# Optimization experiments

Hardware: AMD Instinct MI355X
Metric: run time of the kernel (lower is better)

Reference implementation:

```python
import jax, jax.numpy as jnp
import numpy as np

B, N, K, IN, H, D = 4, 4096, 32, 64, 4, 64  # batch, nodes, max degree, in_dim, heads, out_dim
HD = H * D
NEG_SLOPE = 0.2
EPS = 1e-5


def setup_inputs() -> dict:
    key = jax.random.key(0)
    ks = jax.random.split(key, 10)
    x = jax.random.normal(ks[0], (B, N, IN), jnp.float32)
    # adjacency: each node gets up to K random neighbors (duplicates collapse), no self loops
    nbr = jax.random.randint(ks[1], (B, N, K), 0, N)
    bi = jnp.arange(B)[:, None, None]
    ni = jnp.arange(N)[None, :, None]
    adj = jnp.zeros((B, N, N), jnp.float32).at[bi, ni, nbr].set(1.0)
    adj = adj * (1.0 - jnp.eye(N, dtype=jnp.float32))
    # GATv2Conv params: lin_l / lin_r (both with bias), attention vector att, output bias
    Wl = jax.random.normal(ks[2], (IN, HD), jnp.float32) * 0.05
    bl = jax.random.normal(ks[3], (HD,), jnp.float32) * 0.05
    Wr = jax.random.normal(ks[4], (IN, HD), jnp.float32) * 0.05
    br = jax.random.normal(ks[5], (HD,), jnp.float32) * 0.05
    att = jax.random.normal(ks[6], (H, D), jnp.float32) * 0.05
    bias = jax.random.normal(ks[7], (HD,), jnp.float32) * 0.05
    # LayerNorm params
    gamma = jnp.ones((HD,), jnp.float32)
    beta = jnp.zeros((HD,), jnp.float32)
    return dict(x=x, adj=adj, Wl=Wl, bl=bl, Wr=Wr, br=br, att=att, bias=bias,
                gamma=gamma, beta=beta)


def _gat_layernorm(x, adj, Wl, bl, Wr, br, att, bias, gamma, beta):
    Bx, Nx, _ = x.shape
    # GATv2: x_l from source nodes j, x_r from target nodes i
    xl = (x @ Wl + bl).reshape(Bx, Nx, H, D)
    xr = (x @ Wr + br).reshape(Bx, Nx, H, D)
    # regular neighbor lists from dense adjacency (rows have <= K ones)
    vals, idx = jax.lax.top_k(adj, K)                      # [B,N,K]
    self_idx = jnp.broadcast_to(jnp.arange(Nx)[None, :, None], (Bx, Nx, 1))
    idx_all = jnp.concatenate([idx, self_idx], axis=2)      # [B,N,K+1] (PyG add_self_loops)
    mask = jnp.concatenate([vals > 0, jnp.ones((Bx, Nx, 1), bool)], axis=2)
    # gather source features per edge: [B,N,K+1,H,D]
    xl_j = jax.vmap(lambda t, i: t[i])(xl, idx_all)
    s = jax.nn.leaky_relu(xl_j + xr[:, :, None], NEG_SLOPE)
    e = jnp.einsum('bnkhd,hd->bnkh', s, att)
    e = jnp.where(mask[..., None], e, -jnp.inf)
    alpha = jax.nn.softmax(e, axis=2)                       # segment softmax over neighbors
    out = jnp.einsum('bnkh,bnkhd->bnhd', alpha, xl_j).reshape(Bx, Nx, HD) + bias
    # LayerNorm over H*D
    mu = out.mean(-1, keepdims=True)
    var = ((out - mu) ** 2).mean(-1, keepdims=True)
    return (out - mu) / jnp.sqrt(var + EPS) * gamma + beta


def reference(x, adj, Wl, bl, Wr, br, att, bias, gamma, beta):
    return _gat_layernorm(x, adj, Wl, bl, Wr, br, att, bias, gamma, beta)
```

## Files before the change

kernel.cpp:

```cpp
#include <hip/hip_runtime.h>

#define NN    4096
#define BB    4
#define INDIM 64
#define HD    256
#define KMAX  32
#define SLOTS 33

__global__ __launch_bounds__(256) void xlr_kernel(
    const float* __restrict__ x,
    const float* __restrict__ Wl, const float* __restrict__ bl,
    const float* __restrict__ Wr, const float* __restrict__ br,
    float* __restrict__ XL, float* __restrict__ XR)
{
    __shared__ float xs[INDIM][36];
    const int t = threadIdx.x;
    const int base = blockIdx.x * 32;

    #pragma unroll
    for (int r = 0; r < 2; ++r) {
        float4 xv4 = ((const float4*)x)[(size_t)base * (INDIM / 4) + r * 256 + t];
        int l = (r * 256 + t) * 4;
        int m = l >> 6, c = l & 63;
        xs[c + 0][m] = xv4.x;
        xs[c + 1][m] = xv4.y;
        xs[c + 2][m] = xv4.z;
        xs[c + 3][m] = xv4.w;
    }
    __syncthreads();

    float accl[32], accr[32];
    #pragma unroll
    for (int m = 0; m < 32; ++m) { accl[m] = 0.f; accr[m] = 0.f; }

    for (int c = 0; c < INDIM; ++c) {
        float wl = Wl[c * HD + t];
        float wr = Wr[c * HD + t];
        float xv[32];
        const float4* xp = (const float4*)&xs[c][0];
        float4* dst = (float4*)xv;
        #pragma unroll
        for (int q = 0; q < 8; ++q) dst[q] = xp[q];
        #pragma unroll
        for (int m = 0; m < 32; ++m) {
            accl[m] = fmaf(xv[m], wl, accl[m]);
            accr[m] = fmaf(xv[m], wr, accr[m]);
        }
    }

    float blv = bl[t], brv = br[t];
    #pragma unroll
    for (int m = 0; m < 32; ++m) {
        XL[(size_t)(base + m) * HD + t] = accl[m] + blv;
        XR[(size_t)(base + m) * HD + t] = accr[m] + brv;
    }
}

__global__ __launch_bounds__(256, 3) void gat_kernel(
    const float* __restrict__ adj,
    const float* __restrict__ XL, const float* __restrict__ XR,
    const float* __restrict__ att, const float* __restrict__ bias,
    const float* __restrict__ gamma, const float* __restrict__ beta,
    float* __restrict__ out)
{
    const int node = blockIdx.x;
    const int b    = node >> 12;
    const int i    = node & (NN - 1);
    const int t    = threadIdx.x;
    const int h    = t >> 6;
    const int lane = t & 63;

    __shared__ int   s_nbr[SLOTS];
    __shared__ float s_a[4][SLOTS];
    __shared__ float s_red[4];
    __shared__ int   s_cnt;

    const float xr    = XR[(size_t)node * HD + t];
    const float attv  = att[t];
    const float biasv = bias[t];
    const float gv    = gamma[t];
    const float bv    = beta[t];

    const float4* row = (const float4*)(adj + (size_t)node * NN);
    float4 v[4];
    #pragma unroll
    for (int r = 0; r < 4; ++r) v[r] = row[r * 256 + t];

    if (t == 0) s_cnt = 0;
    __syncthreads();

    #pragma unroll
    for (int r = 0; r < 4; ++r) {
        int j0 = (r * 256 + t) * 4;
        if (v[r].x > 0.f) { int p = atomicAdd(&s_cnt, 1); if (p < KMAX) s_nbr[p] = j0;     }
        if (v[r].y > 0.f) { int p = atomicAdd(&s_cnt, 1); if (p < KMAX) s_nbr[p] = j0 + 1; }
        if (v[r].z > 0.f) { int p = atomicAdd(&s_cnt, 1); if (p < KMAX) s_nbr[p] = j0 + 2; }
        if (v[r].w > 0.f) { int p = atomicAdd(&s_cnt, 1); if (p < KMAX) s_nbr[p] = j0 + 3; }
    }
    __syncthreads();
    int cnt = s_cnt; if (cnt > KMAX) cnt = KMAX;
    if (t >= cnt && t < SLOTS) s_nbr[t] = i;
    __syncthreads();
    const int total = cnt + 1;

    const size_t bbase = (size_t)b * NN * HD;

    float xlv[SLOTS];
    #pragma unroll
    for (int k = 0; k < SLOTS; ++k)
        xlv[k] = XL[bbase + (size_t)s_nbr[k] * HD + t];

    #pragma unroll
    for (int k = 0; k < SLOTS; ++k) {
        float s = xlv[k] + xr;
        s = fmaxf(s, 0.f) + 0.2f * fminf(s, 0.f);
        float c = attv * s;
        #pragma unroll
        for (int off = 32; off; off >>= 1) c += __shfl_xor(c, off);
        if (lane == 0) s_a[h][k] = c;
    }
    __syncthreads();

    float e = (lane < total) ? s_a[h][lane] : -3.0e38f;
    float m = e;
    #pragma unroll
    for (int off = 32; off; off >>= 1) m = fmaxf(m, __shfl_xor(m, off));
    float p = (lane < total) ? __expf(e - m) : 0.f;
    float sm = p;
    #pragma unroll
    for (int off = 32; off; off >>= 1) sm += __shfl_xor(sm, off);
    float alpha = p / sm;
    if (lane < SLOTS) s_a[h][lane] = alpha;
    __syncthreads();

    float acc = 0.f;
    #pragma unroll
    for (int k = 0; k < SLOTS; ++k) acc = fmaf(s_a[h][k], xlv[k], acc);
    acc += biasv;

    float ssum = acc;
    #pragma unroll
    for (int off = 32; off; off >>= 1) ssum += __shfl_xor(ssum, off);
    if (lane == 0) s_red[h] = ssum;
    __syncthreads();
    float mu = (s_red[0] + s_red[1] + s_red[2] + s_red[3]) * (1.f / 256.f);
    __syncthreads();
    float d  = acc - mu;
    float dv = d * d;
    #pragma unroll
    for (int off = 32; off; off >>= 1) dv += __shfl_xor(dv, off);
    if (lane == 0) s_red[h] = dv;
    __syncthreads();
    float var  = (s_red[0] + s_red[1] + s_red[2] + s_red[3]) * (1.f / 256.f);
    float rstd = rsqrtf(var + 1e-5f);
    out[(size_t)node * HD + t] = d * rstd * gv + bv;
}

extern "C" void kernel_launch(void* const* d_in, const int* in_sizes, int n_in,
                              void* d_out, int out_size, void* d_ws, size_t ws_size,
                              hipStream_t stream)
{
    const float* x     = (const float*)d_in[0];
    const float* adj   = (const float*)d_in[1];
    const float* Wl    = (const float*)d_in[2];
    const float* bl    = (const float*)d_in[3];
    const float* Wr    = (const float*)d_in[4];
    const float* br    = (const float*)d_in[5];
    const float* att   = (const float*)d_in[6];
    const float* bias  = (const float*)d_in[7];
    const float* gamma = (const float*)d_in[8];
    const float* beta  = (const float*)d_in[9];
    float* out = (float*)d_out;

    float* XL = (float*)d_ws;
    float* XR = XL + (size_t)BB * NN * HD;

    xlr_kernel<<<BB * NN / 32, 256, 0, stream>>>(x, Wl, bl, Wr, br, XL, XR);
    gat_kernel<<<BB * NN, 256, 0, stream>>>(adj, XL, XR, att, bias, gamma, beta, out);
}
```

Baseline: 499.0 us.

## Use online softmax with per-wave neighbor split in GAT kernel; shrink projection tiles

The GAT kernel is restructured so each of the four waves handles a strided subset of neighbors. Each wave reads the full 256-wide row as float4 (16 lanes per head) and keeps a running max, sum and accumulator, which are merged across waves through shared memory. This replaces the 33-register per-thread gather plus separate softmax and weighted-sum passes, which should cut register pressure and allow four blocks per CU. The projection kernel also moves from 32-row tiles held in shared memory to 4-row tiles read directly from global memory. That raises the block count but reloads the weights more often.

```diff
diff --git a/kernel.cpp b/kernel.cpp
--- a/kernel.cpp
+++ b/kernel.cpp
@@ -7,56 +7,44 @@
 #define KMAX  32
 #define SLOTS 33
 
-__global__ __launch_bounds__(256) void xlr_kernel(
+__global__ __launch_bounds__(256, 4) void xlr_kernel(
     const float* __restrict__ x,
     const float* __restrict__ Wl, const float* __restrict__ bl,
     const float* __restrict__ Wr, const float* __restrict__ br,
     float* __restrict__ XL, float* __restrict__ XR)
 {
-    __shared__ float xs[INDIM][36];
     const int t = threadIdx.x;
-    const int base = blockIdx.x * 32;
+    const int base = blockIdx.x * 4;
+    const float* xp = x + (size_t)base * INDIM;
 
-    #pragma unroll
-    for (int r = 0; r < 2; ++r) {
-        float4 xv4 = ((const float4*)x)[(size_t)base * (INDIM / 4) + r * 256 + t];
-        int l = (r * 256 + t) * 4;
-        int m = l >> 6, c = l & 63;
-        xs[c + 0][m] = xv4.x;
-        xs[c + 1][m] = xv4.y;
-        xs[c + 2][m] = xv4.z;
-        xs[c + 3][m] = xv4.w;
-    }
-    __syncthreads();
+    float al0=0.f, al1=0.f, al2=0.f, al3=0.f;
+    float ar0=0.f, ar1=0.f, ar2=0.f, ar3=0.f;
 
-    float accl[32], accr[32];
-    #pragma unroll
-    for (int m = 0; m < 32; ++m) { accl[m] = 0.f; accr[m] = 0.f; }
-
+    #pragma unroll 8
     for (int c = 0; c < INDIM; ++c) {
         float wl = Wl[c * HD + t];
         float wr = Wr[c * HD + t];
-        float xv[32];
-        const float4* xp = (const float4*)&xs[c][0];
-        float4* dst = (float4*)xv;
-        #pragma unroll
-        for (int q = 0; q < 8; ++q) dst[q] = xp[q];
-        #pragma unroll
-        for (int m = 0; m < 32; ++m) {
-            accl[m] = fmaf(xv[m], wl, accl[m]);
-            accr[m] = fmaf(xv[m], wr, accr[m]);
-        }
+        float x0 = xp[c];
+        float x1 = xp[INDIM + c];
+        float x2 = xp[2 * INDIM + c];
+        float x3 = xp[3 * INDIM + c];
+        al0 = fmaf(x0, wl, al0); ar0 = fmaf(x0, wr, ar0);
+        al1 = fmaf(x1, wl, al1); ar1 = fmaf(x1, wr, ar1);
+        al2 = fmaf(x2, wl, al2); ar2 = fmaf(x2, wr, ar2);
+        al3 = fmaf(x3, wl, al3); ar3 = fmaf(x3, wr, ar3);
     }
-
-    float blv = bl[t], brv = br[t];
-    #pragma unroll
-    for (int m = 0; m < 32; ++m) {
-        XL[(size_t)(base + m) * HD + t] = accl[m] + blv;
-        XR[(size_t)(base + m) * HD + t] = accr[m] + brv;
-    }
+    const float blv = bl[t], brv = br[t];
+    XL[(size_t)(base + 0) * HD + t] = al0 + blv;
+    XL[(size_t)(base + 1) * HD + t] = al1 + blv;
+    XL[(size_t)(base + 2) * HD + t] = al2 + blv;
+    XL[(size_t)(base + 3) * HD + t] = al3 + blv;
+    XR[(size_t)(base + 0) * HD + t] = ar0 + brv;
+    XR[(size_t)(base + 1) * HD + t] = ar1 + brv;
+    XR[(size_t)(base + 2) * HD + t] = ar2 + brv;
+    XR[(size_t)(base + 3) * HD + t] = ar3 + brv;
 }
 
-__global__ __launch_bounds__(256, 3) void gat_kernel(
+__global__ __launch_bounds__(256, 4) void gat_kernel(
     const float* __restrict__ adj,
     const float* __restrict__ XL, const float* __restrict__ XR,
     const float* __restrict__ att, const float* __restrict__ bias,
@@ -67,16 +55,18 @@
     const int b    = node >> 12;
     const int i    = node & (NN - 1);
     const int t    = threadIdx.x;
-    const int h    = t >> 6;
-    const int lane = t & 63;
+    const int w    = t >> 6;
+    const int l    = t & 63;
 
     __shared__ int   s_nbr[SLOTS];
-    __shared__ float s_a[4][SLOTS];
+    __shared__ int   s_cnt;
+    __shared__ float s_acc[4][HD];
+    __shared__ float s_m[4][64];
+    __shared__ float s_s[4][64];
     __shared__ float s_red[4];
-    __shared__ int   s_cnt;
 
-    const float xr    = XR[(size_t)node * HD + t];
-    const float attv  = att[t];
+    const float4 xr4  = *(const float4*)(XR + (size_t)node * HD + 4 * l);
+    const float4 att4 = *(const float4*)(att + 4 * l);
     const float biasv = bias[t];
     const float gv    = gamma[t];
     const float bv    = beta[t];
@@ -105,43 +95,51 @@
 
     const size_t bbase = (size_t)b * NN * HD;
 
-    float xlv[SLOTS];
-    #pragma unroll
-    for (int k = 0; k < SLOTS; ++k)
-        xlv[k] = XL[bbase + (size_t)s_nbr[k] * HD + t];
-
-    #pragma unroll
-    for (int k = 0; k < SLOTS; ++k) {
-        float s = xlv[k] + xr;
-        s = fmaxf(s, 0.f) + 0.2f * fminf(s, 0.f);
-        float c = attv * s;
-        #pragma unroll
-        for (int off = 32; off; off >>= 1) c += __shfl_xor(c, off);
-        if (lane == 0) s_a[h][k] = c;
+    float m = -3.0e38f, s = 0.f;
+    float a0 = 0.f, a1 = 0.f, a2 = 0.f, a3 = 0.f;
+    for (int k = w; k < total; k += 4) {
+        int j = s_nbr[k];
+        float4 q = *(const float4*)(XL + bbase + (size_t)j * HD + 4 * l);
+        float s0 = q.x + xr4.x; s0 = fmaxf(s0, 0.f) + 0.2f * fminf(s0, 0.f);
+        float s1 = q.y + xr4.y; s1 = fmaxf(s1, 0.f) + 0.2f * fminf(s1, 0.f);
+        float s2 = q.z + xr4.z; s2 = fmaxf(s2, 0.f) + 0.2f * fminf(s2, 0.f);
+        float s3 = q.w + xr4.w; s3 = fmaxf(s3, 0.f) + 0.2f * fminf(s3, 0.f);
+        float c = att4.x * s0;
+        c = fmaf(att4.y, s1, c);
+        c = fmaf(att4.z, s2, c);
+        c = fmaf(att4.w, s3, c);
+        c += __shfl_xor(c, 1);
+        c += __shfl_xor(c, 2);
+        c += __shfl_xor(c, 4);
+        c += __shfl_xor(c, 8);
+        float mn    = fmaxf(m, c);
+        float scale = __expf(m - mn);
+        float p     = __expf(c - mn);
+        s  = s * scale + p;
+        a0 = fmaf(p, q.x, a0 * scale);
+        a1 = fmaf(p, q.y, a1 * scale);
+        a2 = fmaf(p, q.z, a2 * scale);
+        a3 = fmaf(p, q.w, a3 * scale);
+        m  = mn;
     }
+    *(float4*)&s_acc[w][4 * l] = make_float4(a0, a1, a2, a3);
+    s_m[w][l] = m;
+    s_s[w][l] = s;
     __syncthreads();
 
-    float e = (lane < total) ? s_a[h][lane] : -3.0e38f;
-    float m = e;
-    #pragma unroll
-    for (int off = 32; off; off >>= 1) m = fmaxf(m, __shfl_xor(m, off));
-    float p = (lane < total) ? __expf(e - m) : 0.f;
-    float sm = p;
-    #pragma unroll
-    for (int off = 32; off; off >>= 1) sm += __shfl_xor(sm, off);
-    float alpha = p / sm;
-    if (lane < SLOTS) s_a[h][lane] = alpha;
-    __syncthreads();
-
-    float acc = 0.f;
-    #pragma unroll
-    for (int k = 0; k < SLOTS; ++k) acc = fmaf(s_a[h][k], xlv[k], acc);
-    acc += biasv;
+    const int g = t >> 2;
+    float m0 = s_m[0][g], m1 = s_m[1][g], m2 = s_m[2][g], m3 = s_m[3][g];
+    float M  = fmaxf(fmaxf(m0, m1), fmaxf(m2, m3));
+    float w0 = __expf(m0 - M), w1 = __expf(m1 - M);
+    float w2 = __expf(m2 - M), w3 = __expf(m3 - M);
+    float den = w0 * s_s[0][g] + w1 * s_s[1][g] + w2 * s_s[2][g] + w3 * s_s[3][g];
+    float num = w0 * s_acc[0][t] + w1 * s_acc[1][t] + w2 * s_acc[2][t] + w3 * s_acc[3][t];
+    float acc = num / den + biasv;
 
     float ssum = acc;
     #pragma unroll
     for (int off = 32; off; off >>= 1) ssum += __shfl_xor(ssum, off);
-    if (lane == 0) s_red[h] = ssum;
+    if (l == 0) s_red[w] = ssum;
     __syncthreads();
     float mu = (s_red[0] + s_red[1] + s_red[2] + s_red[3]) * (1.f / 256.f);
     __syncthreads();
@@ -149,7 +147,7 @@
     float dv = d * d;
     #pragma unroll
     for (int off = 32; off; off >>= 1) dv += __shfl_xor(dv, off);
-    if (lane == 0) s_red[h] = dv;
+    if (l == 0) s_red[w] = dv;
     __syncthreads();
     float var  = (s_red[0] + s_red[1] + s_red[2] + s_red[3]) * (1.f / 256.f);
     float rstd = rsqrtf(var + 1e-5f);
@@ -175,6 +173,6 @@
     float* XL = (float*)d_ws;
     float* XR = XL + (size_t)BB * NN * HD;
 
-    xlr_kernel<<<BB * NN / 32, 256, 0, stream>>>(x, Wl, bl, Wr, br, XL, XR);
+    xlr_kernel<<<BB * NN / 4, 256, 0, stream>>>(x, Wl, bl, Wr, br, XL, XR);
     gat_kernel<<<BB * NN, 256, 0, stream>>>(adj, XL, XR, att, bias, gamma, beta, out);
 }
```

After: 418.9 us. -16.1%, faster.
